# Kernel optimization log

Measured on AMD Instinct MI355X. Metric: run time of the kernel, lower is better.

## Reference

```python
import jax, jax.numpy as jnp
import numpy as np

NUM_HEADS = 8
B, L, D = 4, 1024, 512


def sinusoidal_embeddings(length, dim, decay_term=10000.0):
    positions = jnp.arange(1 - length, length, dtype=jnp.float32).reshape(-1, 1)
    div_term = jnp.exp(-jnp.arange(0, dim, 2, dtype=jnp.float32) * (np.log(decay_term) / dim))
    return jnp.concatenate([jnp.sin(positions * div_term), jnp.cos(positions * div_term)], axis=1)


def setup_inputs() -> dict:
    key = jax.random.key(0)
    k1, k2 = jax.random.split(key)
    x = jax.random.normal(k1, (B, L, D), dtype=jnp.float32)
    W = jax.random.normal(k2, (D, 3 * D), dtype=jnp.float32) * 0.02
    b = jnp.zeros((3 * D,), dtype=jnp.float32)
    return {"x": x, "W": W, "b": b}


def reference(x, W, b):
    batch, length, dim = x.shape
    d_head = dim // NUM_HEADS
    # pointwise Conv(3*dim, kernel_size=1) == dense projection
    proj = jnp.einsum('bld,de->ble', x, W) + b  # [B, L, 3*dim]
    # split heads exactly as the module: reshape to [B,L,H,3*d_head], move heads, split into q,k,v
    proj = proj.reshape(batch, length, NUM_HEADS, 3 * d_head).transpose(0, 2, 1, 3)
    q, k, v = jnp.split(proj, 3, axis=3)  # each [B, H, L, d_head]
    qk = jnp.einsum('bhqd,bhkd->bhqk', q, k)
    # relative position scores via gather (unoptimized path)
    emb_matrix = sinusoidal_embeddings(length, d_head)  # [2L-1, d_head]
    indices = jnp.arange(length)[:, None] - jnp.arange(length) + length - 1  # [L, L]
    embeddings = emb_matrix[indices]  # [L, L, d_head]
    qe = jnp.einsum('bhqd,qkd->bhqk', q, embeddings)
    weights = jax.nn.softmax((qk + qe) / jnp.sqrt(jnp.float32(d_head)), axis=-1)
    output = jnp.einsum('bhqk,bhkd->bhqd', weights, v)
    return output.transpose(0, 2, 1, 3).reshape(batch, length, dim)
```

## Files before the change

kernel.cpp:

```cpp
#include <hip/hip_runtime.h>

typedef unsigned short UST;
typedef __attribute__((ext_vector_type(8))) __bf16 bf16x8;
typedef __attribute__((ext_vector_type(4))) float f32x4;
typedef __attribute__((ext_vector_type(16))) float f32x16;

#define NB 4
#define NH 8
#define LSEQ 1024
#define DMODEL 512
#define DH 64

__device__ __forceinline__ UST f2bf(float f) {
  union { float f; unsigned u; } v; v.f = f;
  unsigned u = v.u;
  return (UST)((u + 0x7FFFu + ((u >> 16) & 1u)) >> 16);
}
__device__ __forceinline__ float bf2f(UST h) {
  union { unsigned u; float f; } v; v.u = ((unsigned)h) << 16;
  return v.f;
}
__device__ __forceinline__ unsigned cvt_pk_bf16(float lo, float hi) {
  unsigned r;
  asm volatile("v_cvt_pk_bf16_f32 %0, %1, %2" : "=v"(r) : "v"(lo), "v"(hi));
  return r;
}

__global__ void k_setup(const float* __restrict__ x, UST* __restrict__ xbf,
                        UST* __restrict__ kext,
                        const float* __restrict__ W, UST* __restrict__ WT) {
  __shared__ float tile[64][65];
  int bid = blockIdx.x;
  if (bid < 2048) {
    int i = bid * 256 + threadIdx.x;
    float4 v = ((const float4*)x)[i];
    ushort4 o;
    o.x = f2bf(v.x); o.y = f2bf(v.y); o.z = f2bf(v.z); o.w = f2bf(v.w);
    ((ushort4*)xbf)[i] = o;
  } else if (bid < 6144) {
    int gid = (bid - 2048) * 256 + threadIdx.x;
    int j = gid & 31;
    int l = (gid >> 5) & 1023;
    int bh = gid >> 15;
    float dd = exp2f((float)(-2 * j) * 0.20762050593046f);
    float ang = (float)l * dd;
    float s = __sinf(ang), c = __cosf(ang);
    UST* kp = kext + ((size_t)bh * 1024 + l) * 128;
    kp[64 + j] = f2bf(c);
    kp[96 + j] = f2bf(s);
  } else {
    int tid = bid - 6144;
    int n0 = (tid % 24) * 64;
    int k0 = (tid / 24) * 64;
    int tx = threadIdx.x & 63, ty = threadIdx.x >> 6;
#pragma unroll
    for (int i = 0; i < 16; ++i) {
      int k = ty + i * 4;
      tile[k][tx] = W[(size_t)(k0 + k) * 1536 + n0 + tx];
    }
    __syncthreads();
#pragma unroll
    for (int i = 0; i < 16; ++i) {
      int n = ty + i * 4;
      WT[(size_t)(n0 + n) * 512 + k0 + tx] = f2bf(tile[tx][n]);
    }
  }
}

__global__ __launch_bounds__(256) void k_proj(
    const UST* __restrict__ xbf, const UST* __restrict__ WT, const float* __restrict__ bias,
    UST* __restrict__ qext, UST* __restrict__ kext, UST* __restrict__ vT) {
  int m0 = blockIdx.x * 128;
  int n0 = blockIdx.y * 64;
  int t = threadIdx.x;
  int lane = t & 63, w = t >> 6;
  int wr = w >> 1, wc = w & 1;
  int g = lane >> 4, c16 = lane & 15;

  __shared__ UST AtS[2][128 * 64];
  __shared__ UST BtS[2][64 * 64];

  const char* Ag = (const char*)(xbf + (size_t)m0 * 512);
  const char* Bg = (const char*)(WT + (size_t)n0 * 512);

  bf16x8 areg[4], breg[2];
#pragma unroll
  for (int c = 0; c < 4; ++c) {
    int u = c * 256 + t, r = u >> 3, s = u & 7;
    areg[c] = *(const bf16x8*)(Ag + (size_t)r * 1024 + s * 16);
  }
#pragma unroll
  for (int c = 0; c < 2; ++c) {
    int u = c * 256 + t, r = u >> 3, s = u & 7;
    breg[c] = *(const bf16x8*)(Bg + (size_t)r * 1024 + s * 16);
  }
#pragma unroll
  for (int c = 0; c < 4; ++c) {
    int u = c * 256 + t, r = u >> 3, s = u & 7;
    *(bf16x8*)((char*)AtS[0] + (size_t)r * 128 + (s ^ (r & 7)) * 16) = areg[c];
  }
#pragma unroll
  for (int c = 0; c < 2; ++c) {
    int u = c * 256 + t, r = u >> 3, s = u & 7;
    *(bf16x8*)((char*)BtS[0] + (size_t)r * 128 + (s ^ (r & 7)) * 16) = breg[c];
  }
#pragma unroll
  for (int c = 0; c < 4; ++c) {
    int u = c * 256 + t, r = u >> 3, s = u & 7;
    areg[c] = *(const bf16x8*)(Ag + (size_t)r * 1024 + 128 + s * 16);
  }
#pragma unroll
  for (int c = 0; c < 2; ++c) {
    int u = c * 256 + t, r = u >> 3, s = u & 7;
    breg[c] = *(const bf16x8*)(Bg + (size_t)r * 1024 + 128 + s * 16);
  }
  __syncthreads();

  f32x4 acc[4][2] = {};
  for (int it = 0; it < 8; ++it) {
    int cur = it & 1;
    const char* Ab = (const char*)(AtS[cur]);
    const char* Bb = (const char*)(BtS[cur]);

#pragma unroll
    for (int kf = 0; kf < 2; ++kf) {
      bf16x8 af[4], bfr[2];
#pragma unroll
      for (int rf = 0; rf < 4; ++rf) {
        int r = wr * 64 + rf * 16 + c16;
        int s = (kf * 4 + g) ^ (r & 7);
        af[rf] = *(const bf16x8*)(Ab + (size_t)r * 128 + s * 16);
      }
#pragma unroll
      for (int cf = 0; cf < 2; ++cf) {
        int r = wc * 32 + cf * 16 + c16;
        int s = (kf * 4 + g) ^ (r & 7);
        bfr[cf] = *(const bf16x8*)(Bb + (size_t)r * 128 + s * 16);
      }
      __builtin_amdgcn_s_setprio(1);
#pragma unroll
      for (int rf = 0; rf < 4; ++rf)
#pragma unroll
        for (int cf = 0; cf < 2; ++cf)
          acc[rf][cf] = __builtin_amdgcn_mfma_f32_16x16x32_bf16(af[rf], bfr[cf], acc[rf][cf], 0, 0, 0);
      __builtin_amdgcn_s_setprio(0);
    }

    if (it < 7) {
      char* Aw = (char*)(AtS[cur ^ 1]);
      char* Bw = (char*)(BtS[cur ^ 1]);
#pragma unroll
      for (int c = 0; c < 4; ++c) {
        int u = c * 256 + t, r = u >> 3, s = u & 7;
        *(bf16x8*)(Aw + (size_t)r * 128 + (s ^ (r & 7)) * 16) = areg[c];
      }
#pragma unroll
      for (int c = 0; c < 2; ++c) {
        int u = c * 256 + t, r = u >> 3, s = u & 7;
        *(bf16x8*)(Bw + (size_t)r * 128 + (s ^ (r & 7)) * 16) = breg[c];
      }
      if (it < 6) {
        size_t cb = (size_t)(it + 2) * 128;
#pragma unroll
        for (int c = 0; c < 4; ++c) {
          int u = c * 256 + t, r = u >> 3, s = u & 7;
          areg[c] = *(const bf16x8*)(Ag + (size_t)r * 1024 + cb + s * 16);
        }
#pragma unroll
        for (int c = 0; c < 2; ++c) {
          int u = c * 256 + t, r = u >> 3, s = u & 7;
          breg[c] = *(const bf16x8*)(Bg + (size_t)r * 1024 + cb + s * 16);
        }
      }
    }
    __syncthreads();
  }

  bool doalpha = (blockIdx.y % 3 == 0);
  UST* stash = AtS[0];

#pragma unroll
  for (int rf = 0; rf < 4; ++rf) {
#pragma unroll
    for (int cf = 0; cf < 2; ++cf) {
      int c = n0 + wc * 32 + cf * 16 + c16;
      int h = c / 192, rem = c % 192;
      float bv = bias[c];
#pragma unroll
      for (int r = 0; r < 4; ++r) {
        int row = m0 + wr * 64 + rf * 16 + g * 4 + r;
        int bidx = row >> 10, ltok = row & 1023;
        int bh = bidx * 8 + h;
        float val = acc[rf][cf][r] + bv;
        if (rem < 64) {
          UST qv = f2bf(val * 0.125f);
          qext[((size_t)bh * 1024 + ltok) * 128 + rem] = qv;
          if (doalpha)
            stash[(size_t)(row - m0) * 64 + rem] = qv;
        } else if (rem < 128)
          kext[((size_t)bh * 1024 + ltok) * 128 + (rem - 64)] = f2bf(val);
        else
          vT[((size_t)bh * 64 + (rem - 128)) * 1024 + ltok] = f2bf(val);
      }
    }
  }

  if (doalpha) {
    __syncthreads();
    int hh = blockIdx.y / 3;
    int rr = t >> 1;
    int row = m0 + rr;
    int bidx = row >> 10, ltok = row & 1023;
    int bh = bidx * 8 + hh;
    UST* qp = qext + ((size_t)bh * 1024 + ltok) * 128;
#pragma unroll
    for (int i = 0; i < 16; ++i) {
      int j = (t & 1) * 16 + i;
      float dd = exp2f((float)(-2 * j) * 0.20762050593046f);
      float ang = (float)ltok * dd;
      float s = __sinf(ang), c = __cosf(ang);
      float qs = bf2f(stash[(size_t)rr * 64 + j]);
      float qc = bf2f(stash[(size_t)rr * 64 + 32 + j]);
      qp[64 + j] = f2bf(qs * s + qc * c);
      qp[96 + j] = f2bf(qc * s - qs * c);
    }
  }
}

__global__ __launch_bounds__(256) void k_attn(
    const UST* __restrict__ qext, const UST* __restrict__ kext,
    const UST* __restrict__ vT, float* __restrict__ out) {
  int blk = ((blockIdx.x & 7) << 6) | (blockIdx.x >> 3);
  int qt = blk & 15, bh = blk >> 4;
  int b = bh >> 3, h = bh & 7;
  int q0 = qt * 64;
  int t = threadIdx.x;
  int lane = t & 63, w = t >> 6;
  int l31 = lane & 31, lh = lane >> 5;
  int wq = w >> 1, wk = w & 1;

  __shared__ UST KtS[2][64 * 128];
  __shared__ UST VtS[2][64 * 64];
  __shared__ float Lsum[2][2][32];

  const UST* qbase = qext + ((size_t)bh * 1024 + q0 + wq * 32 + l31) * 128 + lh * 8;
  bf16x8 qf[8];
#pragma unroll
  for (int c = 0; c < 8; ++c) qf[c] = *(const bf16x8*)&qbase[c * 16];

  const char* kgbase = (const char*)(kext + (size_t)bh * 1024 * 128);
  const char* vgbase = (const char*)(vT + (size_t)bh * 64 * 1024);

  f32x16 O[2] = {};
  float l_lane = 0.f;

  bf16x8 kreg[4], vreg[2];
#pragma unroll
  for (int c = 0; c < 4; ++c) {
    int u = c * 256 + t;
    kreg[c] = *(const bf16x8*)(kgbase + (size_t)(u >> 4) * 256 + (u & 15) * 16);
  }
#pragma unroll
  for (int c = 0; c < 2; ++c) {
    int u = c * 256 + t;
    vreg[c] = *(const bf16x8*)(vgbase + (size_t)(u >> 3) * 2048 + (u & 7) * 16);
  }
#pragma unroll
  for (int c = 0; c < 4; ++c) {
    int u = c * 256 + t, r = u >> 4, s = u & 15;
    *(bf16x8*)((char*)KtS[0] + (size_t)r * 256 + (s ^ ((r ^ (r >> 3)) & 7)) * 16) = kreg[c];
  }
#pragma unroll
  for (int c = 0; c < 2; ++c) {
    int u = c * 256 + t, r = u >> 3, s = u & 7;
    *(bf16x8*)((char*)VtS[0] + (size_t)r * 128 + (s ^ ((r ^ (r >> 3)) & 7)) * 16) = vreg[c];
  }
#pragma unroll
  for (int c = 0; c < 4; ++c) {
    int u = c * 256 + t;
    kreg[c] = *(const bf16x8*)(kgbase + 64 * 256 + (size_t)(u >> 4) * 256 + (u & 15) * 16);
  }
#pragma unroll
  for (int c = 0; c < 2; ++c) {
    int u = c * 256 + t;
    vreg[c] = *(const bf16x8*)(vgbase + 64 * 2 + (size_t)(u >> 3) * 2048 + (u & 7) * 16);
  }
  __syncthreads();

  int krow = wk * 32 + l31;
  int ksalt = (krow ^ (krow >> 3)) & 7;

  for (int it = 0; it < 16; ++it) {
    int cur = it & 1;
    const char* Kb = (const char*)(KtS[cur]);
    const char* Vb = (const char*)(VtS[cur]);

    f32x16 sa = {};
#pragma unroll
    for (int kh = 0; kh < 2; ++kh) {
      bf16x8 kfr[4];
#pragma unroll
      for (int kc = 0; kc < 4; ++kc) {
        int slot = ((kh * 4 + kc) * 2 + lh) ^ ksalt;
        kfr[kc] = *(const bf16x8*)(Kb + (size_t)krow * 256 + slot * 16);
      }
      __builtin_amdgcn_s_setprio(1);
#pragma unroll
      for (int kc = 0; kc < 4; ++kc)
        sa = __builtin_amdgcn_mfma_f32_32x32x16_bf16(kfr[kc], qf[kh * 4 + kc], sa, 0, 0, 0);
      __builtin_amdgcn_s_setprio(0);
    }

    float p[16];
#pragma unroll
    for (int i = 0; i < 16; ++i) {
      p[i] = __expf(sa[i]);
      l_lane += p[i];
    }
    unsigned wv[8], xv[8];
#pragma unroll
    for (int j = 0; j < 8; ++j) wv[j] = cvt_pk_bf16(p[2 * j], p[2 * j + 1]);
#pragma unroll
    for (int j = 0; j < 8; ++j) xv[j] = (unsigned)__shfl_xor((int)wv[j], 32, 64);
    int4 pa0i = lh ? (int4){(int)xv[2], (int)xv[3], (int)wv[2], (int)wv[3]}
                   : (int4){(int)wv[0], (int)wv[1], (int)xv[0], (int)xv[1]};
    int4 pa1i = lh ? (int4){(int)xv[6], (int)xv[7], (int)wv[6], (int)wv[7]}
                   : (int4){(int)wv[4], (int)wv[5], (int)xv[4], (int)xv[5]};
    bf16x8 pa[2] = {*(bf16x8*)&pa0i, *(bf16x8*)&pa1i};

#pragma unroll
    for (int dn = 0; dn < 2; ++dn) {
      int d = dn * 32 + l31;
      int dsalt = (d ^ (d >> 3)) & 7;
      bf16x8 vf[2];
#pragma unroll
      for (int kc = 0; kc < 2; ++kc) {
        int slot = (wk * 4 + kc * 2 + lh) ^ dsalt;
        vf[kc] = *(const bf16x8*)(Vb + (size_t)d * 128 + slot * 16);
      }
      __builtin_amdgcn_s_setprio(1);
#pragma unroll
      for (int kc = 0; kc < 2; ++kc)
        O[dn] = __builtin_amdgcn_mfma_f32_32x32x16_bf16(pa[kc], vf[kc], O[dn], 0, 0, 0);
      __builtin_amdgcn_s_setprio(0);
    }

    if (it < 15) {
      char* Kw = (char*)(KtS[cur ^ 1]);
      char* Vw = (char*)(VtS[cur ^ 1]);
#pragma unroll
      for (int c = 0; c < 4; ++c) {
        int u = c * 256 + t, r = u >> 4, s = u & 15;
        *(bf16x8*)(Kw + (size_t)r * 256 + (s ^ ((r ^ (r >> 3)) & 7)) * 16) = kreg[c];
      }
#pragma unroll
      for (int c = 0; c < 2; ++c) {
        int u = c * 256 + t, r = u >> 3, s = u & 7;
        *(bf16x8*)(Vw + (size_t)r * 128 + (s ^ ((r ^ (r >> 3)) & 7)) * 16) = vreg[c];
      }
      if (it < 14) {
        const char* kg = kgbase + (size_t)(it + 2) * 64 * 256;
#pragma unroll
        for (int c = 0; c < 4; ++c) {
          int u = c * 256 + t;
          kreg[c] = *(const bf16x8*)(kg + (size_t)(u >> 4) * 256 + (u & 15) * 16);
        }
        const char* vg = vgbase + (size_t)(it + 2) * 64 * 2;
#pragma unroll
        for (int c = 0; c < 2; ++c) {
          int u = c * 256 + t;
          vreg[c] = *(const bf16x8*)(vg + (size_t)(u >> 3) * 2048 + (u & 7) * 16);
        }
      }
    }
    __syncthreads();
  }

  l_lane += __shfl_xor(l_lane, 32, 64);
  if (lh == 0) Lsum[wk][wq][l31] = l_lane;
  float* scratch = (float*)KtS[0];
  if (wk == 1) {
#pragma unroll
    for (int i = 0; i < 16; ++i) {
      int qr = wq * 32 + ((i & 3) + 8 * (i >> 2) + 4 * lh);
      scratch[qr * 64 + l31] = O[0][i];
      scratch[qr * 64 + 32 + l31] = O[1][i];
    }
  }
  __syncthreads();
  if (wk == 0) {
#pragma unroll
    for (int i = 0; i < 16; ++i) {
      int cr = (i & 3) + 8 * (i >> 2) + 4 * lh;
      int qr = wq * 32 + cr;
      float inv = 1.0f / (Lsum[0][wq][cr] + Lsum[1][wq][cr]);
      float* op = out + ((size_t)b * 1024 + q0 + qr) * 512 + h * 64;
      op[l31] = (O[0][i] + scratch[qr * 64 + l31]) * inv;
      op[32 + l31] = (O[1][i] + scratch[qr * 64 + 32 + l31]) * inv;
    }
  }
}

extern "C" void kernel_launch(void* const* d_in, const int* in_sizes, int n_in,
                              void* d_out, int out_size, void* d_ws, size_t ws_size,
                              hipStream_t stream) {
  const float* x = (const float*)d_in[0];
  const float* W = (const float*)d_in[1];
  const float* bias = (const float*)d_in[2];
  float* out = (float*)d_out;

  UST* ws = (UST*)d_ws;
  UST* xbf  = ws;
  UST* WT   = xbf + 4096 * 512;
  UST* qext = WT + 1536 * 512;
  UST* kext = qext + 32 * 1024 * 128;
  UST* vT   = kext + 32 * 1024 * 128;

  k_setup<<<dim3(6336), dim3(256), 0, stream>>>(x, xbf, kext, W, WT);
  k_proj<<<dim3(32, 24), dim3(256), 0, stream>>>(xbf, WT, bias, qext, kext, vT);
  k_attn<<<dim3(512), dim3(256), 0, stream>>>(qext, kext, vT, out);
}
```

Before: 54.11 us.

## Split attention over the key dimension and add a partial-sum combine kernel

The attention kernel is templated on a split count. With two splits, each block processes half of the key/value tiles and writes unnormalized partial outputs and row sums to workspace. A new combine kernel then adds the partials and normalizes. This doubles the number of attention blocks to improve CU occupancy, at the cost of extra global traffic for the fp32 partials and one more kernel launch. The split path is chosen only when the workspace is large enough.

Measured after the change: 59.11 us. +9.3%, slower.

```diff
diff --git a/kernel.cpp b/kernel.cpp
--- a/kernel.cpp
+++ b/kernel.cpp
@@ -227,10 +227,13 @@
   }
 }
 
-__global__ __launch_bounds__(256) void k_attn(
+template<int SPLITS>
+__global__ __launch_bounds__(256) void k_attn_split(
     const UST* __restrict__ qext, const UST* __restrict__ kext,
-    const UST* __restrict__ vT, float* __restrict__ out) {
+    const UST* __restrict__ vT, float* __restrict__ out,
+    float* __restrict__ Opart, float* __restrict__ lpart) {
   int blk = ((blockIdx.x & 7) << 6) | (blockIdx.x >> 3);
+  int split = blockIdx.y;
   int qt = blk & 15, bh = blk >> 4;
   int b = bh >> 3, h = bh & 7;
   int q0 = qt * 64;
@@ -239,6 +242,9 @@
   int l31 = lane & 31, lh = lane >> 5;
   int wq = w >> 1, wk = w & 1;
 
+  const int ITERS = 16 / SPLITS;
+  int tile0 = split * ITERS;
+
   __shared__ UST KtS[2][64 * 128];
   __shared__ UST VtS[2][64 * 64];
   __shared__ float Lsum[2][2][32];
@@ -248,8 +254,8 @@
 #pragma unroll
   for (int c = 0; c < 8; ++c) qf[c] = *(const bf16x8*)&qbase[c * 16];
 
-  const char* kgbase = (const char*)(kext + (size_t)bh * 1024 * 128);
-  const char* vgbase = (const char*)(vT + (size_t)bh * 64 * 1024);
+  const char* kgbase = (const char*)(kext + (size_t)bh * 1024 * 128) + (size_t)tile0 * 64 * 256;
+  const char* vgbase = (const char*)(vT + (size_t)bh * 64 * 1024) + (size_t)tile0 * 64 * 2;
 
   f32x16 O[2] = {};
   float l_lane = 0.f;
@@ -290,7 +296,7 @@
   int krow = wk * 32 + l31;
   int ksalt = (krow ^ (krow >> 3)) & 7;
 
-  for (int it = 0; it < 16; ++it) {
+  for (int it = 0; it < ITERS; ++it) {
     int cur = it & 1;
     const char* Kb = (const char*)(KtS[cur]);
     const char* Vb = (const char*)(VtS[cur]);
@@ -345,7 +351,7 @@
       __builtin_amdgcn_s_setprio(0);
     }
 
-    if (it < 15) {
+    if (it < ITERS - 1) {
       char* Kw = (char*)(KtS[cur ^ 1]);
       char* Vw = (char*)(VtS[cur ^ 1]);
 #pragma unroll
@@ -358,7 +364,7 @@
         int u = c * 256 + t, r = u >> 3, s = u & 7;
         *(bf16x8*)(Vw + (size_t)r * 128 + (s ^ ((r ^ (r >> 3)) & 7)) * 16) = vreg[c];
       }
-      if (it < 14) {
+      if (it < ITERS - 2) {
         const char* kg = kgbase + (size_t)(it + 2) * 64 * 256;
 #pragma unroll
         for (int c = 0; c < 4; ++c) {
@@ -393,12 +399,43 @@
     for (int i = 0; i < 16; ++i) {
       int cr = (i & 3) + 8 * (i >> 2) + 4 * lh;
       int qr = wq * 32 + cr;
-      float inv = 1.0f / (Lsum[0][wq][cr] + Lsum[1][wq][cr]);
-      float* op = out + ((size_t)b * 1024 + q0 + qr) * 512 + h * 64;
-      op[l31] = (O[0][i] + scratch[qr * 64 + l31]) * inv;
-      op[32 + l31] = (O[1][i] + scratch[qr * 64 + 32 + l31]) * inv;
-    }
-  }
+      float lsumv = Lsum[0][wq][cr] + Lsum[1][wq][cr];
+      if (SPLITS == 1) {
+        float inv = 1.0f / lsumv;
+        float* op = out + ((size_t)b * 1024 + q0 + qr) * 512 + h * 64;
+        op[l31] = (O[0][i] + scratch[qr * 64 + l31]) * inv;
+        op[32 + l31] = (O[1][i] + scratch[qr * 64 + 32 + l31]) * inv;
+      } else {
+        float* op = Opart + (((size_t)split * 32 + bh) * 1024 + q0 + qr) * 64;
+        op[l31] = O[0][i] + scratch[qr * 64 + l31];
+        op[32 + l31] = O[1][i] + scratch[qr * 64 + 32 + l31];
+        if (l31 == 0)
+          lpart[((size_t)split * 32 + bh) * 1024 + q0 + qr] = lsumv;
+      }
+    }
+  }
+}
+
+template<int PARTS>
+__global__ void k_combine(const float* __restrict__ Opart, const float* __restrict__ lpart,
+                          float* __restrict__ out) {
+  int gid = blockIdx.x * 256 + threadIdx.x;
+  int dq = (gid & 15) * 4;
+  int row = (gid >> 4) & 1023;
+  int bh = gid >> 14;
+  int b = bh >> 3, h = bh & 7;
+
+  float denom = 0.f;
+  float4 acc = {0.f, 0.f, 0.f, 0.f};
+#pragma unroll
+  for (int s = 0; s < PARTS; ++s) {
+    denom += lpart[((size_t)s * 32 + bh) * 1024 + row];
+    float4 ov = *(const float4*)&Opart[(((size_t)s * 32 + bh) * 1024 + row) * 64 + dq];
+    acc.x += ov.x; acc.y += ov.y; acc.z += ov.z; acc.w += ov.w;
+  }
+  float inv = 1.0f / denom;
+  float4 o = {acc.x * inv, acc.y * inv, acc.z * inv, acc.w * inv};
+  *(float4*)&out[((size_t)b * 1024 + row) * 512 + h * 64 + dq] = o;
 }
 
 extern "C" void kernel_launch(void* const* d_in, const int* in_sizes, int n_in,
@@ -415,8 +452,22 @@
   UST* qext = WT + 1536 * 512;
   UST* kext = qext + 32 * 1024 * 128;
   UST* vT   = kext + 32 * 1024 * 128;
+  UST* bf_end = vT + 32 * 64 * 1024;
+
+  size_t base_bytes = (size_t)(bf_end - ws) * sizeof(UST);
+  size_t opart_bytes = (size_t)2 * 32 * 1024 * 64 * sizeof(float);
+  size_t lpart_bytes = (size_t)2 * 32 * 1024 * sizeof(float);
+  int S = (ws_size >= base_bytes + opart_bytes + lpart_bytes) ? 2 : 1;
+
+  float* Opart = (float*)bf_end;
+  float* lpart = Opart + (size_t)2 * 32 * 1024 * 64;
 
   k_setup<<<dim3(6336), dim3(256), 0, stream>>>(x, xbf, kext, W, WT);
   k_proj<<<dim3(32, 24), dim3(256), 0, stream>>>(xbf, WT, bias, qext, kext, vT);
-  k_attn<<<dim3(512), dim3(256), 0, stream>>>(qext, kext, vT, out);
-}
+  if (S == 2) {
+    k_attn_split<2><<<dim3(512, 2), dim3(256), 0, stream>>>(qext, kext, vT, out, Opart, lpart);
+    k_combine<2><<<dim3(2048), dim3(256), 0, stream>>>(Opart, lpart, out);
+  } else {
+    k_attn_split<1><<<dim3(512, 1), dim3(256), 0, stream>>>(qext, kext, vT, out, Opart, lpart);
+  }
+}
```
